# Kernel tuning notes

Measured on AMD Instinct MI355X. Metric: run time of the kernel, lower is better.

Reference implementation:

```python
import jax, jax.numpy as jnp
import numpy as np

EPS = 1e-5  # BatchNorm eps

def _gcn_norm(edge_index, edge_weight, n):
    # PyG gcn_norm with add_self_loops=True, fill_value=1.0
    loop = jnp.arange(n, dtype=edge_index.dtype)
    row = jnp.concatenate([edge_index[0], loop])
    col = jnp.concatenate([edge_index[1], loop])
    ew = jnp.concatenate([edge_weight, jnp.ones((n,), edge_weight.dtype)])
    deg = jax.ops.segment_sum(ew, col, num_segments=n)
    dis = jnp.where(deg > 0, jax.lax.rsqrt(jnp.maximum(deg, 1e-30)), 0.0)
    norm = dis[row] * ew * dis[col]
    return row, col, norm

def _gcn_conv(x, W, b, row, col, norm, n):
    h = x @ W                               # [N, out]
    msg = h[row] * norm[:, None]            # gather + edge scale
    out = jax.ops.segment_sum(msg, col, num_segments=n)
    return out + b

def _bn_eval(x, gamma, beta, mean, var):
    return (x - mean) * jax.lax.rsqrt(var + EPS) * gamma + beta

def setup_inputs() -> dict:
    key = jax.random.key(0)
    ks = jax.random.split(key, 12)
    N, E, V, H = 100000, 1600000, 256, 128
    x = jax.random.normal(ks[0], (N, V), jnp.float32)
    edge_index = jax.random.randint(ks[1], (2, E), 0, N, jnp.int64)
    edge_weight = jax.random.uniform(ks[2], (E,), jnp.float32)
    s = lambda fan: 1.0 / np.sqrt(fan)
    return {
        "x": x, "edge_index": edge_index, "edge_weight": edge_weight,
        "W1": jax.random.normal(ks[3], (V, H), jnp.float32) * s(V),
        "b1": jnp.zeros((H,), jnp.float32),
        "W2": jax.random.normal(ks[4], (H, H), jnp.float32) * s(H),
        "b2": jnp.zeros((H,), jnp.float32),
        "W3": jax.random.normal(ks[5], (H, 1), jnp.float32) * s(H),
        "b3": jnp.zeros((1,), jnp.float32),
        "Wres": jax.random.normal(ks[6], (V, H), jnp.float32) * s(V),
        "g1": jnp.ones((H,), jnp.float32), "be1": jnp.zeros((H,), jnp.float32),
        "m1": jax.random.normal(ks[7], (H,), jnp.float32) * 0.01,
        "v1": jnp.ones((H,), jnp.float32),
        "g2": jnp.ones((H,), jnp.float32), "be2": jnp.zeros((H,), jnp.float32),
        "m2": jax.random.normal(ks[8], (H,), jnp.float32) * 0.01,
        "v2": jnp.ones((H,), jnp.float32),
    }

def reference(x, edge_index, edge_weight, W1, b1, W2, b2, W3, b3, Wres,
              g1, be1, m1, v1, g2, be2, m2, v2):
    n = x.shape[0]
    row, col, norm = _gcn_norm(edge_index, edge_weight, n)
    res = x @ Wres                                   # residual branch
    h = _gcn_conv(x, W1, b1, row, col, norm, n)
    h = jax.nn.relu(_bn_eval(h, g1, be1, m1, v1))    # dropout off (eval)
    h = _gcn_conv(h, W2, b2, row, col, norm, n) + res
    h = jax.nn.relu(_bn_eval(h, g2, be2, m2, v2))
    h = _gcn_conv(h, W3, b3, row, col, norm, n)      # [N, 1]
    return jnp.squeeze(h, axis=1)
```

## Files before the change

kernel.cpp:

```cpp
#include <hip/hip_runtime.h>
#include <hip/hip_bf16.h>

#define BN_EPS 1e-5f

using short8 = __attribute__((ext_vector_type(8))) short;
using f32x4  = __attribute__((ext_vector_type(4))) float;

#define FIX_SCALE 1048576.0f
#define FIX_MASK  ((1ULL << 42) - 1)
#define CNT_ONE   (1ULL << 42)

static __device__ __forceinline__ unsigned short f2bf(float f) {
  unsigned int u = __float_as_uint(f);
  unsigned int r = (u + 0x7fffu + ((u >> 16) & 1u)) >> 16;
  return (unsigned short)r;
}


static __global__ void cast_weights(const float* __restrict__ W1, const float* __restrict__ Wres,
                                    const float* __restrict__ W2,
                                    unsigned short* __restrict__ BT1,
                                    unsigned short* __restrict__ BT2) {
  int i = blockIdx.x * blockDim.x + threadIdx.x;
  if (i < 256 * 256) {
    int n = i >> 8, k = i & 255;
    float v = (n < 128) ? W1[k * 128 + n] : Wres[k * 128 + (n - 128)];
    BT1[i] = f2bf(v);
  } else if (i < 256 * 256 + 128 * 128) {
    int j = i - 256 * 256;
    int n = j >> 7, k = j & 127;
    BT2[j] = f2bf(W2[k * 128 + n]);
  }
}


static __global__ __launch_bounds__(256)
void fused_gemm1_hist(const float* __restrict__ A, const unsigned short* __restrict__ BT,
                      unsigned short* __restrict__ C0, float* __restrict__ C1, int M,
                      const int* __restrict__ col, const float* __restrict__ ew,
                      unsigned long long* __restrict__ packed,
                      unsigned short* __restrict__ rank, int E, int gemmBlocks) {
  __shared__ unsigned short As[64 * 40];
  __shared__ unsigned short Bs[256 * 40];

  if (blockIdx.x >= gemmBlocks) {
    int e = (blockIdx.x - gemmBlocks) * blockDim.x + threadIdx.x;
    if (e < E) {
      int c = col[e];
      unsigned long long fx = (unsigned long long)(unsigned int)(ew[e] * FIX_SCALE + 0.5f);
      unsigned long long old = atomicAdd(&packed[c], CNT_ONE | fx);
      rank[e] = (unsigned short)(old >> 42);
    }
    return;
  }

  int t = threadIdx.x;
  int wv = t >> 6, lane = t & 63;
  int quad = lane >> 4, l15 = lane & 15;
  int m0 = blockIdx.x * 64;

  f32x4 acc[4][4];
#pragma unroll
  for (int i = 0; i < 4; ++i)
#pragma unroll
    for (int j = 0; j < 4; ++j) acc[i][j] = (f32x4){0.f, 0.f, 0.f, 0.f};

  int ar = t >> 2;
  int ac = (t & 3) * 8;
  bool avalid = (m0 + ar) < M;
  const float* Arow = A + (size_t)(m0 + ar) * 256 + ac;
  const unsigned short* Brow = BT + (size_t)t * 256;

  for (int k0 = 0; k0 < 256; k0 += 32) {
    float4 a0 = make_float4(0.f, 0.f, 0.f, 0.f), a1 = a0;
    if (avalid) {
      a0 = *(const float4*)(Arow + k0);
      a1 = *(const float4*)(Arow + k0 + 4);
    }
    short8 av;
    av[0] = (short)f2bf(a0.x); av[1] = (short)f2bf(a0.y);
    av[2] = (short)f2bf(a0.z); av[3] = (short)f2bf(a0.w);
    av[4] = (short)f2bf(a1.x); av[5] = (short)f2bf(a1.y);
    av[6] = (short)f2bf(a1.z); av[7] = (short)f2bf(a1.w);
    *(short8*)&As[ar * 40 + ac] = av;

    short8 b0 = *(const short8*)(Brow + k0);
    short8 b1 = *(const short8*)(Brow + k0 + 8);
    short8 b2 = *(const short8*)(Brow + k0 + 16);
    short8 b3 = *(const short8*)(Brow + k0 + 24);
    *(short8*)&Bs[t * 40 + 0]  = b0;
    *(short8*)&Bs[t * 40 + 8]  = b1;
    *(short8*)&Bs[t * 40 + 16] = b2;
    *(short8*)&Bs[t * 40 + 24] = b3;
    __syncthreads();

    short8 af[4], bf[4];
#pragma unroll
    for (int mt = 0; mt < 4; ++mt)
      af[mt] = *(const short8*)&As[(mt * 16 + l15) * 40 + quad * 8];
#pragma unroll
    for (int nt = 0; nt < 4; ++nt)
      bf[nt] = *(const short8*)&Bs[(wv * 64 + nt * 16 + l15) * 40 + quad * 8];
#pragma unroll
    for (int mt = 0; mt < 4; ++mt)
#pragma unroll
      for (int nt = 0; nt < 4; ++nt)
        acc[mt][nt] = __builtin_amdgcn_mfma_f32_16x16x32_bf16(af[mt], bf[nt], acc[mt][nt], 0, 0, 0);
    __syncthreads();
  }

  int nbase = wv * 64;
#pragma unroll
  for (int mt = 0; mt < 4; ++mt) {
#pragma unroll
    for (int nt = 0; nt < 4; ++nt) {
      int n = nbase + nt * 16 + l15;
#pragma unroll
      for (int reg = 0; reg < 4; ++reg) {
        size_t m = (size_t)(m0 + mt * 16 + quad * 4 + reg);
        if (nbase < 128) C0[m * 128 + n] = f2bf(acc[mt][nt][reg]);
        else             C1[m * 128 + (n - 128)] = acc[mt][nt][reg];
      }
    }
  }
}


#define SCAN_B 256
#define SCAN_I 4
static __global__ void scanA(const unsigned long long* __restrict__ packed,
                             float* __restrict__ dis, int* __restrict__ cnt,
                             int* __restrict__ start, int* __restrict__ blkSum, int N) {
  __shared__ int sh[SCAN_B];
  int t = threadIdx.x;
  int base = blockIdx.x * SCAN_B * SCAN_I + t * SCAN_I;
  int v[SCAN_I];
  int tot = 0;
#pragma unroll
  for (int j = 0; j < SCAN_I; ++j) {
    if (base + j < N) {
      unsigned long long pv = packed[base + j];
      v[j] = (int)(pv >> 42);
      cnt[base + j] = v[j];
      float deg = 1.0f + (float)(pv & FIX_MASK) * (1.0f / FIX_SCALE);
      dis[base + j] = rsqrtf(deg);
    } else v[j] = 0;
    tot += v[j];
  }
  sh[t] = tot;
  __syncthreads();
  int self = tot;
  for (int off = 1; off < SCAN_B; off <<= 1) {
    int add = (t >= off) ? sh[t - off] : 0;
    __syncthreads();
    sh[t] += add;
    __syncthreads();
  }
  int excl = sh[t] - self;
  if (t == SCAN_B - 1) blkSum[blockIdx.x] = sh[t];
  int run = excl;
#pragma unroll
  for (int j = 0; j < SCAN_I; ++j) {
    if (base + j < N) start[base + j] = run;
    run += v[j];
  }
}

static __global__ void scanB(const int* __restrict__ blkSum, int* __restrict__ blkOff, int nb) {
  __shared__ int sh[256];
  int t = threadIdx.x;
  int v = (t < nb) ? blkSum[t] : 0;
  sh[t] = v;
  __syncthreads();
  for (int off = 1; off < 256; off <<= 1) {
    int add = (t >= off) ? sh[t - off] : 0;
    __syncthreads();
    sh[t] += add;
    __syncthreads();
  }
  if (t < nb) blkOff[t] = sh[t] - v;
}

static __global__ void scanC(int* start, const int* __restrict__ blkOff, int N) {
  int i = blockIdx.x * blockDim.x + threadIdx.x;
  if (i < N) start[i] += blkOff[i / (SCAN_B * SCAN_I)];
}

static __global__ void place_kernel(const int* __restrict__ row, const int* __restrict__ col,
                                    const float* __restrict__ ew, const float* __restrict__ dis,
                                    const int* __restrict__ start,
                                    const unsigned short* __restrict__ rank,
                                    long long* __restrict__ edges, int E) {
  int e = blockIdx.x * blockDim.x + threadIdx.x;
  if (e < E) {
    int r = row[e], c = col[e];
    int pos = start[c] + (int)rank[e];
    float nrm = dis[r] * ew[e];
    long long v = ((long long)__float_as_int(nrm) << 32) | (unsigned int)r;
    __builtin_nontemporal_store(v, &edges[pos]);
  }
}


static __global__ __launch_bounds__(256)
void gemm2_mfma(const unsigned short* __restrict__ A, const unsigned short* __restrict__ BT,
                unsigned short* __restrict__ C, int Mp) {
  __shared__ unsigned short As[128 * 40];
  __shared__ unsigned short Bs[128 * 40];
  int t = threadIdx.x;
  int wv = t >> 6, lane = t & 63;
  int quad = lane >> 4, l15 = lane & 15;
  int m0 = blockIdx.x * 128;

  f32x4 acc[4][4];
#pragma unroll
  for (int i = 0; i < 4; ++i)
#pragma unroll
    for (int j = 0; j < 4; ++j) acc[i][j] = (f32x4){0.f, 0.f, 0.f, 0.f};

  int sr = t >> 1, sc = (t & 1) * 16;

  for (int k0 = 0; k0 < 128; k0 += 32) {
    short8 a0 = *(const short8*)(A + (size_t)(m0 + sr) * 128 + k0 + sc);
    short8 a1 = *(const short8*)(A + (size_t)(m0 + sr) * 128 + k0 + sc + 8);
    *(short8*)&As[sr * 40 + sc]     = a0;
    *(short8*)&As[sr * 40 + sc + 8] = a1;
    short8 b0 = *(const short8*)(BT + (size_t)sr * 128 + k0 + sc);
    short8 b1 = *(const short8*)(BT + (size_t)sr * 128 + k0 + sc + 8);
    *(short8*)&Bs[sr * 40 + sc]     = b0;
    *(short8*)&Bs[sr * 40 + sc + 8] = b1;
    __syncthreads();

    int mb = (wv >> 1) * 64, nb = (wv & 1) * 64;
    short8 af[4], bf[4];
#pragma unroll
    for (int mt = 0; mt < 4; ++mt)
      af[mt] = *(const short8*)&As[(mb + mt * 16 + l15) * 40 + quad * 8];
#pragma unroll
    for (int nt = 0; nt < 4; ++nt)
      bf[nt] = *(const short8*)&Bs[(nb + nt * 16 + l15) * 40 + quad * 8];
#pragma unroll
    for (int mt = 0; mt < 4; ++mt)
#pragma unroll
      for (int nt = 0; nt < 4; ++nt)
        acc[mt][nt] = __builtin_amdgcn_mfma_f32_16x16x32_bf16(af[mt], bf[nt], acc[mt][nt], 0, 0, 0);
    __syncthreads();
  }

  int mb = (wv >> 1) * 64, nb = (wv & 1) * 64;
#pragma unroll
  for (int mt = 0; mt < 4; ++mt)
#pragma unroll
    for (int nt = 0; nt < 4; ++nt) {
      int n = nb + nt * 16 + l15;
#pragma unroll
      for (int reg = 0; reg < 4; ++reg) {
        size_t m = (size_t)(m0 + mb + mt * 16 + quad * 4 + reg);
        C[m * 128 + n] = f2bf(acc[mt][nt][reg]);
      }
    }
  (void)Mp;
}


#define PROP_GATHER_BODY                                                        \
  int c0 = lane * 2;                                                            \
  float d = dis[w];                                                             \
  float acc0, acc1;                                                             \
  {                                                                             \
    unsigned int u = Hsrc[(size_t)w * 64 + lane];                               \
    acc0 = d * __uint_as_float(u << 16);                                        \
    acc1 = d * __uint_as_float(u & 0xffff0000u);                                \
  }                                                                             \
  int s = start[w], n = cnt[w];                                                 \
  int k = 0;                                                                    \
  while (k < n) {                                                               \
    int chunk = min(n - k, 64);                                                 \
    int idx = 0;                                                                \
    float wt = 0.f;                                                             \
    if (lane < chunk) {                                                         \
      long long ev = edges[s + k + lane];                                       \
      idx = (int)(unsigned int)(ev & 0xffffffffLL);                             \
      wt  = __int_as_float((int)(ev >> 32));                                    \
    }                                                                           \
    for (int j = 0; j < chunk; j += 8) {                                        \
      int   i0 = __shfl(idx, j + 0, 64), i1 = __shfl(idx, j + 1, 64);           \
      int   i2 = __shfl(idx, j + 2, 64), i3 = __shfl(idx, j + 3, 64);           \
      int   i4 = __shfl(idx, j + 4, 64), i5 = __shfl(idx, j + 5, 64);           \
      int   i6 = __shfl(idx, j + 6, 64), i7 = __shfl(idx, j + 7, 64);           \
      float w0 = __shfl(wt, j + 0, 64), w1 = __shfl(wt, j + 1, 64);             \
      float w2 = __shfl(wt, j + 2, 64), w3 = __shfl(wt, j + 3, 64);             \
      float w4 = __shfl(wt, j + 4, 64), w5 = __shfl(wt, j + 5, 64);             \
      float w6 = __shfl(wt, j + 6, 64), w7 = __shfl(wt, j + 7, 64);             \
      unsigned int u0 = Hsrc[(size_t)i0 * 64 + lane];                           \
      unsigned int u1 = Hsrc[(size_t)i1 * 64 + lane];                           \
      unsigned int u2 = Hsrc[(size_t)i2 * 64 + lane];                           \
      unsigned int u3 = Hsrc[(size_t)i3 * 64 + lane];                           \
      unsigned int u4 = Hsrc[(size_t)i4 * 64 + lane];                           \
      unsigned int u5 = Hsrc[(size_t)i5 * 64 + lane];                           \
      unsigned int u6 = Hsrc[(size_t)i6 * 64 + lane];                           \
      unsigned int u7 = Hsrc[(size_t)i7 * 64 + lane];                           \
      acc0 = fmaf(w0, __uint_as_float(u0 << 16), acc0);                         \
      acc1 = fmaf(w0, __uint_as_float(u0 & 0xffff0000u), acc1);                 \
      acc0 = fmaf(w1, __uint_as_float(u1 << 16), acc0);                         \
      acc1 = fmaf(w1, __uint_as_float(u1 & 0xffff0000u), acc1);                 \
      acc0 = fmaf(w2, __uint_as_float(u2 << 16), acc0);                         \
      acc1 = fmaf(w2, __uint_as_float(u2 & 0xffff0000u), acc1);                 \
      acc0 = fmaf(w3, __uint_as_float(u3 << 16), acc0);                         \
      acc1 = fmaf(w3, __uint_as_float(u3 & 0xffff0000u), acc1);                 \
      acc0 = fmaf(w4, __uint_as_float(u4 << 16), acc0);                         \
      acc1 = fmaf(w4, __uint_as_float(u4 & 0xffff0000u), acc1);                 \
      acc0 = fmaf(w5, __uint_as_float(u5 << 16), acc0);                         \
      acc1 = fmaf(w5, __uint_as_float(u5 & 0xffff0000u), acc1);                 \
      acc0 = fmaf(w6, __uint_as_float(u6 << 16), acc0);                         \
      acc1 = fmaf(w6, __uint_as_float(u6 & 0xffff0000u), acc1);                 \
      acc0 = fmaf(w7, __uint_as_float(u7 << 16), acc0);                         \
      acc1 = fmaf(w7, __uint_as_float(u7 & 0xffff0000u), acc1);                 \
    }                                                                           \
    k += chunk;                                                                 \
  }                                                                             \
  acc0 *= d;                                                                    \
  acc1 *= d;

static __global__ __launch_bounds__(256)
void prop128_bf16out(const unsigned int* __restrict__ Hsrc,
                     const int* __restrict__ start, const int* __restrict__ cnt,
                     const long long* __restrict__ edges,
                     const float* __restrict__ dis,
                     const float* __restrict__ bvec,
                     const float* __restrict__ g, const float* __restrict__ be,
                     const float* __restrict__ mean, const float* __restrict__ var,
                     unsigned int* __restrict__ Outb, int N) {
  int w = (int)((blockIdx.x * blockDim.x + threadIdx.x) >> 6);
  int lane = threadIdx.x & 63;
  if (w >= N) return;
  PROP_GATHER_BODY
  float x0 = acc0 + bvec[c0];
  float x1 = acc1 + bvec[c0 + 1];
  float s0 = g[c0] * rsqrtf(var[c0] + BN_EPS);
  float s1 = g[c0 + 1] * rsqrtf(var[c0 + 1] + BN_EPS);
  x0 = fmaxf((x0 - mean[c0]) * s0 + be[c0], 0.f);
  x1 = fmaxf((x1 - mean[c0 + 1]) * s1 + be[c0 + 1], 0.f);
  unsigned int packed = (unsigned int)f2bf(x0) | ((unsigned int)f2bf(x1) << 16);
  Outb[(size_t)w * 64 + lane] = packed;
}

static __global__ __launch_bounds__(256)
void prop128_w3out(const unsigned int* __restrict__ Hsrc,
                   const int* __restrict__ start, const int* __restrict__ cnt,
                   const long long* __restrict__ edges,
                   const float* __restrict__ dis,
                   const float* __restrict__ bvec,
                   const float* __restrict__ g, const float* __restrict__ be,
                   const float* __restrict__ mean, const float* __restrict__ var,
                   const float* __restrict__ res, const float* __restrict__ W3,
                   float* __restrict__ h3, int N) {
  int w = (int)((blockIdx.x * blockDim.x + threadIdx.x) >> 6);
  int lane = threadIdx.x & 63;
  if (w >= N) return;
  PROP_GATHER_BODY
  float x0 = acc0 + bvec[c0] + res[(size_t)w * 128 + c0];
  float x1 = acc1 + bvec[c0 + 1] + res[(size_t)w * 128 + c0 + 1];
  float s0 = g[c0] * rsqrtf(var[c0] + BN_EPS);
  float s1 = g[c0 + 1] * rsqrtf(var[c0 + 1] + BN_EPS);
  x0 = fmaxf((x0 - mean[c0]) * s0 + be[c0], 0.f);
  x1 = fmaxf((x1 - mean[c0 + 1]) * s1 + be[c0 + 1], 0.f);
  float v = x0 * W3[c0] + x1 * W3[c0 + 1];
#pragma unroll
  for (int off = 32; off > 0; off >>= 1) v += __shfl_down(v, off, 64);
  if (lane == 0) h3[w] = v;
}


static __global__ void prop3_kernel(const float* __restrict__ h3,
                                    const int* __restrict__ start, const int* __restrict__ cnt,
                                    const long long* __restrict__ edges,
                                    const float* __restrict__ dis, const float* __restrict__ b3,
                                    float* __restrict__ out, int N) {
  int i = blockIdx.x * blockDim.x + threadIdx.x;
  if (i >= N) return;
  float d = dis[i];
  float acc = d * h3[i];
  int s = start[i], n = cnt[i];
  for (int k = 0; k < n; ++k) {
    long long ev = edges[s + k];
    int src = (int)(unsigned int)(ev & 0xffffffffLL);
    float wt = __int_as_float((int)(ev >> 32));
    acc = fmaf(wt, h3[src], acc);
  }
  out[i] = acc * d + b3[0];
}


extern "C" void kernel_launch(void* const* d_in, const int* in_sizes, int n_in,
                              void* d_out, int out_size, void* d_ws, size_t ws_size,
                              hipStream_t stream) {
  const float* x    = (const float*)d_in[0];
  const int*   ei   = (const int*)d_in[1];
  const float* ew   = (const float*)d_in[2];
  const float* W1   = (const float*)d_in[3];
  const float* b1   = (const float*)d_in[4];
  const float* W2   = (const float*)d_in[5];
  const float* b2   = (const float*)d_in[6];
  const float* W3   = (const float*)d_in[7];
  const float* b3   = (const float*)d_in[8];
  const float* Wres = (const float*)d_in[9];
  const float* g1   = (const float*)d_in[10];
  const float* be1  = (const float*)d_in[11];
  const float* m1   = (const float*)d_in[12];
  const float* v1   = (const float*)d_in[13];
  const float* g2   = (const float*)d_in[14];
  const float* be2  = (const float*)d_in[15];
  const float* m2   = (const float*)d_in[16];
  const float* v2   = (const float*)d_in[17];

  int Hh = in_sizes[4];
  int V  = in_sizes[3] / Hh;
  int N  = in_sizes[0] / V;
  int E  = in_sizes[2];
  const int* row = ei;
  const int* col = ei + E;

  int Mp = ((N + 127) / 128) * 128;

  char* p = (char*)d_ws;
  auto alloc = [&](size_t bytes) -> char* {
    char* r = p;
    p += (bytes + 255) & ~(size_t)255;
    return r;
  };
  unsigned long long* packed = (unsigned long long*)alloc((size_t)N * 8);
  float* dis    = (float*)alloc((size_t)N * 4);
  int*   cnt    = (int*)  alloc((size_t)N * 4);
  int*   startA = (int*)  alloc((size_t)N * 4);
  int*   blkSum = (int*)  alloc(256 * 4);
  int*   blkOff = (int*)  alloc(256 * 4);
  unsigned short* rank = (unsigned short*)alloc((size_t)E * 2);
  long long* edges = (long long*)alloc((size_t)E * 8);
  float* h3     = (float*)alloc((size_t)N * 4);
  unsigned short* BT1 = (unsigned short*)alloc((size_t)256 * 256 * 2);
  unsigned short* BT2 = (unsigned short*)alloc((size_t)128 * 128 * 2);
  unsigned short* bufG  = (unsigned short*)alloc((size_t)Mp * 128 * 2);
  unsigned short* bufH1 = (unsigned short*)alloc((size_t)Mp * 128 * 2);
  float* bufRes = (float*)alloc((size_t)Mp * 128 * 4);
  (void)ws_size; (void)n_in; (void)out_size;

  int TB = 256;
  hipMemsetAsync(packed, 0, (size_t)N * 8, stream);
  cast_weights<<<(256 * 256 + 128 * 128 + TB - 1) / TB, TB, 0, stream>>>(W1, Wres, W2, BT1, BT2);

  int gB = Mp / 64;
  int hB = (E + TB - 1) / TB;
  fused_gemm1_hist<<<gB + hB, TB, 0, stream>>>(x, BT1, bufG, bufRes, N,
                                               col, ew, packed, rank, E, gB);

  int nb = (N + SCAN_B * SCAN_I - 1) / (SCAN_B * SCAN_I);
  scanA<<<nb, SCAN_B, 0, stream>>>(packed, dis, cnt, startA, blkSum, N);
  scanB<<<1, 256, 0, stream>>>(blkSum, blkOff, nb);
  scanC<<<(N + TB - 1) / TB, TB, 0, stream>>>(startA, blkOff, N);
  place_kernel<<<(E + TB - 1) / TB, TB, 0, stream>>>(row, col, ew, dis, startA, rank, edges, E);

  int propBlocks = (int)(((size_t)N * 64 + TB - 1) / TB);
  prop128_bf16out<<<propBlocks, TB, 0, stream>>>((const unsigned int*)bufG, startA, cnt,
                                                 edges, dis, b1, g1, be1, m1, v1,
                                                 (unsigned int*)bufH1, N);

  gemm2_mfma<<<Mp / 128, 256, 0, stream>>>(bufH1, BT2, bufG, Mp);

  prop128_w3out<<<propBlocks, TB, 0, stream>>>((const unsigned int*)bufG, startA, cnt,
                                               edges, dis, b2, g2, be2, m2, v2,
                                               bufRes, W3, h3, N);

  prop3_kernel<<<(N + TB - 1) / TB, TB, 0, stream>>>(h3, startA, cnt, edges,
                                                     dis, b3, (float*)d_out, N);
}
```

Baseline: 503.9 us.

## Partition degree histogram across copies and drop LDS staging in GEMMs

The edge degree histogram now spreads its atomics over eight partitioned copies chosen by block index. This is meant to reduce atomic contention on a single counter per node. The scan merges the partitions and writes per-partition offsets that place_kernel adds to the edge position. Both MFMA GEMMs now load operand fragments straight from global memory into registers with no shared-memory tiles or barriers, and the A conversion uses a cheaper bf16 packing (round-half-up rather than round-to-even). The cost is a larger memset, extra scan reads, and redundant global loads in the GEMMs, which now rely on cache reuse.

```diff
diff --git a/kernel.cpp b/kernel.cpp
--- a/kernel.cpp
+++ b/kernel.cpp
@@ -9,11 +9,18 @@
 #define FIX_SCALE 1048576.0f
 #define FIX_MASK  ((1ULL << 42) - 1)
 #define CNT_ONE   (1ULL << 42)
+#define NPART 8
 
 static __device__ __forceinline__ unsigned short f2bf(float f) {
   unsigned int u = __float_as_uint(f);
   unsigned int r = (u + 0x7fffu + ((u >> 16) & 1u)) >> 16;
   return (unsigned short)r;
+}
+
+static __device__ __forceinline__ unsigned int pkbf(float x, float y) {
+  unsigned int a = (__float_as_uint(x) + 0x8000u) >> 16;
+  unsigned int b = (__float_as_uint(y) + 0x8000u) & 0xffff0000u;
+  return a | b;
 }
 
 
@@ -38,17 +45,15 @@
 void fused_gemm1_hist(const float* __restrict__ A, const unsigned short* __restrict__ BT,
                       unsigned short* __restrict__ C0, float* __restrict__ C1, int M,
                       const int* __restrict__ col, const float* __restrict__ ew,
-                      unsigned long long* __restrict__ packed,
-                      unsigned short* __restrict__ rank, int E, int gemmBlocks) {
-  __shared__ unsigned short As[64 * 40];
-  __shared__ unsigned short Bs[256 * 40];
-
+                      unsigned long long* __restrict__ packedH,
+                      unsigned short* __restrict__ rank, int E, int gemmBlocks, int N) {
   if (blockIdx.x >= gemmBlocks) {
     int e = (blockIdx.x - gemmBlocks) * blockDim.x + threadIdx.x;
     if (e < E) {
       int c = col[e];
+      int part = blockIdx.x & (NPART - 1);
       unsigned long long fx = (unsigned long long)(unsigned int)(ew[e] * FIX_SCALE + 0.5f);
-      unsigned long long old = atomicAdd(&packed[c], CNT_ONE | fx);
+      unsigned long long old = atomicAdd(&packedH[(size_t)part * N + c], CNT_ONE | fx);
       rank[e] = (unsigned short)(old >> 42);
     }
     return;
@@ -58,6 +63,7 @@
   int wv = t >> 6, lane = t & 63;
   int quad = lane >> 4, l15 = lane & 15;
   int m0 = blockIdx.x * 64;
+  int nbase = wv * 64;
 
   f32x4 acc[4][4];
 #pragma unroll
@@ -65,51 +71,42 @@
 #pragma unroll
     for (int j = 0; j < 4; ++j) acc[i][j] = (f32x4){0.f, 0.f, 0.f, 0.f};
 
-  int ar = t >> 2;
-  int ac = (t & 3) * 8;
-  bool avalid = (m0 + ar) < M;
-  const float* Arow = A + (size_t)(m0 + ar) * 256 + ac;
-  const unsigned short* Brow = BT + (size_t)t * 256;
-
-  for (int k0 = 0; k0 < 256; k0 += 32) {
-    float4 a0 = make_float4(0.f, 0.f, 0.f, 0.f), a1 = a0;
-    if (avalid) {
-      a0 = *(const float4*)(Arow + k0);
-      a1 = *(const float4*)(Arow + k0 + 4);
+  const float* Aptr[4];
+#pragma unroll
+  for (int mt = 0; mt < 4; ++mt) {
+    int m = m0 + mt * 16 + l15;
+    if (m >= M) m = M - 1;
+    Aptr[mt] = A + (size_t)m * 256 + quad * 8;
+  }
+  const unsigned short* Bptr[4];
+#pragma unroll
+  for (int nt = 0; nt < 4; ++nt)
+    Bptr[nt] = BT + (size_t)(nbase + nt * 16 + l15) * 256 + quad * 8;
+
+#pragma unroll
+  for (int kk = 0; kk < 8; ++kk) {
+    short8 af[4], bf[4];
+#pragma unroll
+    for (int mt = 0; mt < 4; ++mt) {
+      float4 a0 = *(const float4*)(Aptr[mt] + kk * 32);
+      float4 a1 = *(const float4*)(Aptr[mt] + kk * 32 + 4);
+      int4 pa;
+      pa.x = (int)pkbf(a0.x, a0.y);
+      pa.y = (int)pkbf(a0.z, a0.w);
+      pa.z = (int)pkbf(a1.x, a1.y);
+      pa.w = (int)pkbf(a1.z, a1.w);
+      af[mt] = *(short8*)&pa;
     }
-    short8 av;
-    av[0] = (short)f2bf(a0.x); av[1] = (short)f2bf(a0.y);
-    av[2] = (short)f2bf(a0.z); av[3] = (short)f2bf(a0.w);
-    av[4] = (short)f2bf(a1.x); av[5] = (short)f2bf(a1.y);
-    av[6] = (short)f2bf(a1.z); av[7] = (short)f2bf(a1.w);
-    *(short8*)&As[ar * 40 + ac] = av;
-
-    short8 b0 = *(const short8*)(Brow + k0);
-    short8 b1 = *(const short8*)(Brow + k0 + 8);
-    short8 b2 = *(const short8*)(Brow + k0 + 16);
-    short8 b3 = *(const short8*)(Brow + k0 + 24);
-    *(short8*)&Bs[t * 40 + 0]  = b0;
-    *(short8*)&Bs[t * 40 + 8]  = b1;
-    *(short8*)&Bs[t * 40 + 16] = b2;
-    *(short8*)&Bs[t * 40 + 24] = b3;
-    __syncthreads();
-
-    short8 af[4], bf[4];
-#pragma unroll
-    for (int mt = 0; mt < 4; ++mt)
-      af[mt] = *(const short8*)&As[(mt * 16 + l15) * 40 + quad * 8];
 #pragma unroll
     for (int nt = 0; nt < 4; ++nt)
-      bf[nt] = *(const short8*)&Bs[(wv * 64 + nt * 16 + l15) * 40 + quad * 8];
+      bf[nt] = *(const short8*)(Bptr[nt] + kk * 32);
 #pragma unroll
     for (int mt = 0; mt < 4; ++mt)
 #pragma unroll
       for (int nt = 0; nt < 4; ++nt)
         acc[mt][nt] = __builtin_amdgcn_mfma_f32_16x16x32_bf16(af[mt], bf[nt], acc[mt][nt], 0, 0, 0);
-    __syncthreads();
-  }
-
-  int nbase = wv * 64;
+  }
+
 #pragma unroll
   for (int mt = 0; mt < 4; ++mt) {
 #pragma unroll
@@ -128,7 +125,8 @@
 
 #define SCAN_B 256
 #define SCAN_I 4
-static __global__ void scanA(const unsigned long long* __restrict__ packed,
+static __global__ void scanA(const unsigned long long* __restrict__ packedH,
+                             int* __restrict__ pofs,
                              float* __restrict__ dis, int* __restrict__ cnt,
                              int* __restrict__ start, int* __restrict__ blkSum, int N) {
   __shared__ int sh[SCAN_B];
@@ -139,11 +137,20 @@
 #pragma unroll
   for (int j = 0; j < SCAN_I; ++j) {
     if (base + j < N) {
-      unsigned long long pv = packed[base + j];
-      v[j] = (int)(pv >> 42);
-      cnt[base + j] = v[j];
-      float deg = 1.0f + (float)(pv & FIX_MASK) * (1.0f / FIX_SCALE);
-      dis[base + j] = rsqrtf(deg);
+      int i = base + j;
+      int cum = 0;
+      unsigned long long fix = 0;
+#pragma unroll
+      for (int p = 0; p < NPART; ++p) {
+        unsigned long long pv = packedH[(size_t)p * N + i];
+        pofs[(size_t)p * N + i] = cum;
+        cum += (int)(pv >> 42);
+        fix += pv & FIX_MASK;
+      }
+      v[j] = cum;
+      cnt[i] = cum;
+      float deg = 1.0f + (float)fix * (1.0f / FIX_SCALE);
+      dis[i] = rsqrtf(deg);
     } else v[j] = 0;
     tot += v[j];
   }
@@ -189,12 +196,14 @@
 static __global__ void place_kernel(const int* __restrict__ row, const int* __restrict__ col,
                                     const float* __restrict__ ew, const float* __restrict__ dis,
                                     const int* __restrict__ start,
+                                    const int* __restrict__ pofs,
                                     const unsigned short* __restrict__ rank,
-                                    long long* __restrict__ edges, int E) {
+                                    long long* __restrict__ edges, int E, int gB, int N) {
   int e = blockIdx.x * blockDim.x + threadIdx.x;
   if (e < E) {
     int r = row[e], c = col[e];
-    int pos = start[c] + (int)rank[e];
+    int part = (gB + (e >> 8)) & (NPART - 1);
+    int pos = start[c] + pofs[(size_t)part * N + c] + (int)rank[e];
     float nrm = dis[r] * ew[e];
     long long v = ((long long)__float_as_int(nrm) << 32) | (unsigned int)r;
     __builtin_nontemporal_store(v, &edges[pos]);
@@ -204,13 +213,12 @@
 
 static __global__ __launch_bounds__(256)
 void gemm2_mfma(const unsigned short* __restrict__ A, const unsigned short* __restrict__ BT,
-                unsigned short* __restrict__ C, int Mp) {
-  __shared__ unsigned short As[128 * 40];
-  __shared__ unsigned short Bs[128 * 40];
+                unsigned short* __restrict__ C) {
   int t = threadIdx.x;
   int wv = t >> 6, lane = t & 63;
   int quad = lane >> 4, l15 = lane & 15;
   int m0 = blockIdx.x * 128;
+  int mb = (wv >> 1) * 64, nb = (wv & 1) * 64;
 
   f32x4 acc[4][4];
 #pragma unroll
@@ -218,36 +226,29 @@
 #pragma unroll
     for (int j = 0; j < 4; ++j) acc[i][j] = (f32x4){0.f, 0.f, 0.f, 0.f};
 
-  int sr = t >> 1, sc = (t & 1) * 16;
-
-  for (int k0 = 0; k0 < 128; k0 += 32) {
-    short8 a0 = *(const short8*)(A + (size_t)(m0 + sr) * 128 + k0 + sc);
-    short8 a1 = *(const short8*)(A + (size_t)(m0 + sr) * 128 + k0 + sc + 8);
-    *(short8*)&As[sr * 40 + sc]     = a0;
-    *(short8*)&As[sr * 40 + sc + 8] = a1;
-    short8 b0 = *(const short8*)(BT + (size_t)sr * 128 + k0 + sc);
-    short8 b1 = *(const short8*)(BT + (size_t)sr * 128 + k0 + sc + 8);
-    *(short8*)&Bs[sr * 40 + sc]     = b0;
-    *(short8*)&Bs[sr * 40 + sc + 8] = b1;
-    __syncthreads();
-
-    int mb = (wv >> 1) * 64, nb = (wv & 1) * 64;
+  const unsigned short* Aptr[4];
+  const unsigned short* Bptr[4];
+#pragma unroll
+  for (int mt = 0; mt < 4; ++mt)
+    Aptr[mt] = A + (size_t)(m0 + mb + mt * 16 + l15) * 128 + quad * 8;
+#pragma unroll
+  for (int nt = 0; nt < 4; ++nt)
+    Bptr[nt] = BT + (size_t)(nb + nt * 16 + l15) * 128 + quad * 8;
+
+#pragma unroll
+  for (int kk = 0; kk < 4; ++kk) {
     short8 af[4], bf[4];
 #pragma unroll
-    for (int mt = 0; mt < 4; ++mt)
-      af[mt] = *(const short8*)&As[(mb + mt * 16 + l15) * 40 + quad * 8];
-#pragma unroll
-    for (int nt = 0; nt < 4; ++nt)
-      bf[nt] = *(const short8*)&Bs[(nb + nt * 16 + l15) * 40 + quad * 8];
+    for (int mt = 0; mt < 4; ++mt) af[mt] = *(const short8*)(Aptr[mt] + kk * 32);
+#pragma unroll
+    for (int nt = 0; nt < 4; ++nt) bf[nt] = *(const short8*)(Bptr[nt] + kk * 32);
 #pragma unroll
     for (int mt = 0; mt < 4; ++mt)
 #pragma unroll
       for (int nt = 0; nt < 4; ++nt)
         acc[mt][nt] = __builtin_amdgcn_mfma_f32_16x16x32_bf16(af[mt], bf[nt], acc[mt][nt], 0, 0, 0);
-    __syncthreads();
-  }
-
-  int mb = (wv >> 1) * 64, nb = (wv & 1) * 64;
+  }
+
 #pragma unroll
   for (int mt = 0; mt < 4; ++mt)
 #pragma unroll
@@ -259,7 +260,6 @@
         C[m * 128 + n] = f2bf(acc[mt][nt][reg]);
       }
     }
-  (void)Mp;
 }
 
 
@@ -429,7 +429,8 @@
     p += (bytes + 255) & ~(size_t)255;
     return r;
   };
-  unsigned long long* packed = (unsigned long long*)alloc((size_t)N * 8);
+  unsigned long long* packedH = (unsigned long long*)alloc((size_t)NPART * N * 8);
+  int*   pofs   = (int*)  alloc((size_t)NPART * N * 4);
   float* dis    = (float*)alloc((size_t)N * 4);
   int*   cnt    = (int*)  alloc((size_t)N * 4);
   int*   startA = (int*)  alloc((size_t)N * 4);
@@ -446,26 +447,27 @@
   (void)ws_size; (void)n_in; (void)out_size;
 
   int TB = 256;
-  hipMemsetAsync(packed, 0, (size_t)N * 8, stream);
+  hipMemsetAsync(packedH, 0, (size_t)NPART * N * 8, stream);
   cast_weights<<<(256 * 256 + 128 * 128 + TB - 1) / TB, TB, 0, stream>>>(W1, Wres, W2, BT1, BT2);
 
   int gB = Mp / 64;
   int hB = (E + TB - 1) / TB;
   fused_gemm1_hist<<<gB + hB, TB, 0, stream>>>(x, BT1, bufG, bufRes, N,
-                                               col, ew, packed, rank, E, gB);
+                                               col, ew, packedH, rank, E, gB, N);
 
   int nb = (N + SCAN_B * SCAN_I - 1) / (SCAN_B * SCAN_I);
-  scanA<<<nb, SCAN_B, 0, stream>>>(packed, dis, cnt, startA, blkSum, N);
+  scanA<<<nb, SCAN_B, 0, stream>>>(packedH, pofs, dis, cnt, startA, blkSum, N);
   scanB<<<1, 256, 0, stream>>>(blkSum, blkOff, nb);
   scanC<<<(N + TB - 1) / TB, TB, 0, stream>>>(startA, blkOff, N);
-  place_kernel<<<(E + TB - 1) / TB, TB, 0, stream>>>(row, col, ew, dis, startA, rank, edges, E);
+  place_kernel<<<(E + TB - 1) / TB, TB, 0, stream>>>(row, col, ew, dis, startA, pofs,
+                                                     rank, edges, E, gB, N);
 
   int propBlocks = (int)(((size_t)N * 64 + TB - 1) / TB);
   prop128_bf16out<<<propBlocks, TB, 0, stream>>>((const unsigned int*)bufG, startA, cnt,
                                                  edges, dis, b1, g1, be1, m1, v1,
                                                  (unsigned int*)bufH1, N);
 
-  gemm2_mfma<<<Mp / 128, 256, 0, stream>>>(bufH1, BT2, bufG, Mp);
+  gemm2_mfma<<<Mp / 128, 256, 0, stream>>>(bufH1, BT2, bufG);
 
   prop128_w3out<<<propBlocks, TB, 0, stream>>>((const unsigned int*)bufG, startA, cnt,
                                                edges, dis, b2, g2, be2, m2, v2,
```

New measurement: 550.6 us. 1.09x slower.

## Store residual in bf16 and interleave GEMM blocks with histogram blocks

Applied to the files above, without the earlier changes.

The residual branch output is now written as bf16 instead of fp32, which halves its write in the first GEMM and its read in the second propagation kernel. The fused GEMM+histogram launch also spreads GEMM blocks evenly among histogram blocks (one GEMM block every R blocks) instead of running all GEMM blocks first, so compute-heavy and atomic-heavy work overlap across CUs. The residual loses precision to bf16 rounding, and the interleaved block-index mapping adds a little integer arithmetic per block.

```diff
diff --git a/kernel.cpp b/kernel.cpp
--- a/kernel.cpp
+++ b/kernel.cpp
@@ -36,15 +36,21 @@
 
 static __global__ __launch_bounds__(256)
 void fused_gemm1_hist(const float* __restrict__ A, const unsigned short* __restrict__ BT,
-                      unsigned short* __restrict__ C0, float* __restrict__ C1, int M,
+                      unsigned short* __restrict__ C0, unsigned short* __restrict__ C1, int M,
                       const int* __restrict__ col, const float* __restrict__ ew,
                       unsigned long long* __restrict__ packed,
-                      unsigned short* __restrict__ rank, int E, int gemmBlocks) {
+                      unsigned short* __restrict__ rank, int E, int gB, int R) {
   __shared__ unsigned short As[64 * 40];
   __shared__ unsigned short Bs[256 * 40];
 
-  if (blockIdx.x >= gemmBlocks) {
-    int e = (blockIdx.x - gemmBlocks) * blockDim.x + threadIdx.x;
+  int b = blockIdx.x;
+  int g = b / R;
+  bool isGemm = (b % R == 0) && (g < gB);
+
+  if (!isGemm) {
+    int nGemmBefore = min((b + R - 1) / R, gB);
+    int histIdx = b - nGemmBefore;
+    int e = histIdx * blockDim.x + threadIdx.x;
     if (e < E) {
       int c = col[e];
       unsigned long long fx = (unsigned long long)(unsigned int)(ew[e] * FIX_SCALE + 0.5f);
@@ -57,7 +63,7 @@
   int t = threadIdx.x;
   int wv = t >> 6, lane = t & 63;
   int quad = lane >> 4, l15 = lane & 15;
-  int m0 = blockIdx.x * 64;
+  int m0 = g * 64;
 
   f32x4 acc[4][4];
 #pragma unroll
@@ -119,7 +125,7 @@
       for (int reg = 0; reg < 4; ++reg) {
         size_t m = (size_t)(m0 + mt * 16 + quad * 4 + reg);
         if (nbase < 128) C0[m * 128 + n] = f2bf(acc[mt][nt][reg]);
-        else             C1[m * 128 + (n - 128)] = acc[mt][nt][reg];
+        else             C1[m * 128 + (n - 128)] = f2bf(acc[mt][nt][reg]);
       }
     }
   }
@@ -204,7 +210,7 @@
 
 static __global__ __launch_bounds__(256)
 void gemm2_mfma(const unsigned short* __restrict__ A, const unsigned short* __restrict__ BT,
-                unsigned short* __restrict__ C, int Mp) {
+                unsigned short* __restrict__ C) {
   __shared__ unsigned short As[128 * 40];
   __shared__ unsigned short Bs[128 * 40];
   int t = threadIdx.x;
@@ -259,7 +265,6 @@
         C[m * 128 + n] = f2bf(acc[mt][nt][reg]);
       }
     }
-  (void)Mp;
 }
 
 
@@ -353,14 +358,15 @@
                    const float* __restrict__ bvec,
                    const float* __restrict__ g, const float* __restrict__ be,
                    const float* __restrict__ mean, const float* __restrict__ var,
-                   const float* __restrict__ res, const float* __restrict__ W3,
+                   const unsigned int* __restrict__ resb, const float* __restrict__ W3,
                    float* __restrict__ h3, int N) {
   int w = (int)((blockIdx.x * blockDim.x + threadIdx.x) >> 6);
   int lane = threadIdx.x & 63;
   if (w >= N) return;
   PROP_GATHER_BODY
-  float x0 = acc0 + bvec[c0] + res[(size_t)w * 128 + c0];
-  float x1 = acc1 + bvec[c0 + 1] + res[(size_t)w * 128 + c0 + 1];
+  unsigned int ru = resb[(size_t)w * 64 + lane];
+  float x0 = acc0 + bvec[c0]     + __uint_as_float(ru << 16);
+  float x1 = acc1 + bvec[c0 + 1] + __uint_as_float(ru & 0xffff0000u);
   float s0 = g[c0] * rsqrtf(var[c0] + BN_EPS);
   float s1 = g[c0 + 1] * rsqrtf(var[c0 + 1] + BN_EPS);
   x0 = fmaxf((x0 - mean[c0]) * s0 + be[c0], 0.f);
@@ -442,7 +448,7 @@
   unsigned short* BT2 = (unsigned short*)alloc((size_t)128 * 128 * 2);
   unsigned short* bufG  = (unsigned short*)alloc((size_t)Mp * 128 * 2);
   unsigned short* bufH1 = (unsigned short*)alloc((size_t)Mp * 128 * 2);
-  float* bufRes = (float*)alloc((size_t)Mp * 128 * 4);
+  unsigned short* bufRes = (unsigned short*)alloc((size_t)Mp * 128 * 2);
   (void)ws_size; (void)n_in; (void)out_size;
 
   int TB = 256;
@@ -451,25 +457,28 @@
 
   int gB = Mp / 64;
   int hB = (E + TB - 1) / TB;
-  fused_gemm1_hist<<<gB + hB, TB, 0, stream>>>(x, BT1, bufG, bufRes, N,
-                                               col, ew, packed, rank, E, gB);
+  int total = gB + hB;
+  int R = total / gB;
+  fused_gemm1_hist<<<total, TB, 0, stream>>>(x, BT1, bufG, bufRes, N,
+                                             col, ew, packed, rank, E, gB, R);
 
   int nb = (N + SCAN_B * SCAN_I - 1) / (SCAN_B * SCAN_I);
   scanA<<<nb, SCAN_B, 0, stream>>>(packed, dis, cnt, startA, blkSum, N);
   scanB<<<1, 256, 0, stream>>>(blkSum, blkOff, nb);
   scanC<<<(N + TB - 1) / TB, TB, 0, stream>>>(startA, blkOff, N);
-  place_kernel<<<(E + TB - 1) / TB, TB, 0, stream>>>(row, col, ew, dis, startA, rank, edges, E);
+  place_kernel<<<(E + TB - 1) / TB, TB, 0, stream>>>(row, col, ew, dis, startA,
+                                                     rank, edges, E);
 
   int propBlocks = (int)(((size_t)N * 64 + TB - 1) / TB);
   prop128_bf16out<<<propBlocks, TB, 0, stream>>>((const unsigned int*)bufG, startA, cnt,
                                                  edges, dis, b1, g1, be1, m1, v1,
                                                  (unsigned int*)bufH1, N);
 
-  gemm2_mfma<<<Mp / 128, 256, 0, stream>>>(bufH1, BT2, bufG, Mp);
+  gemm2_mfma<<<Mp / 128, 256, 0, stream>>>(bufH1, BT2, bufG);
 
   prop128_w3out<<<propBlocks, TB, 0, stream>>>((const unsigned int*)bufG, startA, cnt,
                                                edges, dis, b2, g2, be2, m2, v2,
-                                               bufRes, W3, h3, N);
+                                               (const unsigned int*)bufRes, W3, h3, N);
 
   prop3_kernel<<<(N + TB - 1) / TB, TB, 0, stream>>>(h3, startA, cnt, edges,
                                                      dis, b3, (float*)d_out, N);
```

New measurement: 625.3 us. +24.1%, slower.
